# Kernel optimization log

Measured on AMD Instinct MI355X. Metric: run time of the kernel, lower is better.

The kernel has to match this reference:

```python
import jax, jax.numpy as jnp
import numpy as np

N = 100000        # n_nodes
E = 1600000       # n_edges (avg degree 16)
D = 64            # latent_dim_S
H = 64            # gcn_hidden_dim
EPS = 1e-5        # BatchNorm1d eps


def setup_inputs() -> dict:
    key = jax.random.key(0)
    ks = jax.random.split(key, 6)
    return {
        "edge_index": jax.random.randint(ks[0], (2, E), 0, N, dtype=jnp.int64),
        "u_S": jax.random.normal(ks[1], (N, D), dtype=jnp.float32),
        # GCNConv 1: latent_dim_S -> gcn_hidden_dim
        "w1": jax.random.normal(ks[2], (D, H), dtype=jnp.float32) / np.sqrt(D).astype(np.float32),
        "b1": jnp.zeros((H,), jnp.float32),
        # BatchNorm1d(H)
        "g1": jnp.ones((H,), jnp.float32),
        "beta1": jnp.zeros((H,), jnp.float32),
        # GCNConv 2: gcn_hidden_dim -> 2
        "w2": jax.random.normal(ks[3], (H, 2), dtype=jnp.float32) / np.sqrt(H).astype(np.float32),
        "b2": jnp.zeros((2,), jnp.float32),
        # BatchNorm1d(2)
        "g2": jnp.ones((2,), jnp.float32),
        "beta2": jnp.zeros((2,), jnp.float32),
    }


def reference(edge_index, u_S, w1, b1, g1, beta1, w2, b2, g2, beta2):
    n = u_S.shape[0]
    # PyG GCNConv: add self-loops, symmetric normalization D^-1/2 A D^-1/2
    loop = jnp.arange(n, dtype=edge_index.dtype)
    src = jnp.concatenate([edge_index[0], loop])  # [E+N]
    dst = jnp.concatenate([edge_index[1], loop])
    deg = jnp.zeros((n,), u_S.dtype).at[dst].add(1.0)   # in-degree incl. self-loop (>=1)
    dinv = jax.lax.rsqrt(deg)
    norm = dinv[src] * dinv[dst]                         # [E+N]

    def gcn_conv(x, w, b):
        h = x @ w                                        # transform first (PyG order)
        msg = h[src] * norm[:, None]                     # gather + scale
        out = jnp.zeros((n, h.shape[1]), h.dtype).at[dst].add(msg)  # scatter-add
        return out + b                                   # bias after aggregation

    def batchnorm(x, g, bt):
        m = x.mean(axis=0)
        v = x.var(axis=0)                                # biased variance (train mode)
        return g * (x - m) * jax.lax.rsqrt(v + EPS) + bt

    s = jax.nn.relu(batchnorm(gcn_conv(u_S, w1, b1), g1, beta1))
    s = batchnorm(gcn_conv(s, w2, b2), g2, beta2)
    # nn.Softmax() on 2D input defaults to dim=1
    return jax.nn.sigmoid(s), jax.nn.softmax(s, axis=1)
```

## Files before the change

### kernel.cpp

```cpp
#include <hip/hip_runtime.h>
#include <hip/hip_fp16.h>

#define N_NODES 100000
#define N_EDGES 1600000
#define BN_EPS 1e-5f

#define NBUCK 256
#define NPB   391
#define BCAP  8192
#define EPB_BIN 4096
#define NBLK_BIN ((N_EDGES + EPB_BIN - 1) / EPB_BIN)

#define K7_NBLK 1563

#define OFF_GCUR   0
#define OFF_CNT    256
#define OFF_DINV   100352
#define OFF_OFFS   200448
#define OFF_EBUF   300544
#define OFF_STATS1 2397696
#define OFF_STATS2 2397824
#define OFF_HS1    2398016
#define OFF_BINNED OFF_HS1
#define OFF_OUT1   5598016
#define OFF_HS2    8798016
#define OFF_OUT2   8998016

typedef _Float16 f16x8 __attribute__((ext_vector_type(8)));
typedef float    f32x4 __attribute__((ext_vector_type(4)));

__device__ inline void cvt8(uint4 v, float* f) {
    float2 a = __half22float2(*(__half2*)&v.x);
    float2 b = __half22float2(*(__half2*)&v.y);
    float2 c = __half22float2(*(__half2*)&v.z);
    float2 d = __half22float2(*(__half2*)&v.w);
    f[0] = a.x; f[1] = a.y; f[2] = b.x; f[3] = b.y;
    f[4] = c.x; f[5] = c.y; f[6] = d.x; f[7] = d.y;
}

__global__ __launch_bounds__(256) void k0_init(int* __restrict__ gcur,
                                               float* __restrict__ stats) {
    int t = threadIdx.x;
    gcur[t] = t * BCAP;
    if (t < 132) stats[t] = 0.f;
}

__global__ __launch_bounds__(256) void k_bin(
        const int* __restrict__ src, const int* __restrict__ dst,
        int* __restrict__ gcur, int* __restrict__ binned) {
    __shared__ int hist[NBUCK];
    __shared__ int lcur[NBUCK];
    int t = threadIdx.x, b = blockIdx.x;
    hist[t] = 0;
    __syncthreads();
    int e0 = b * EPB_BIN;
    int pkreg[16], bkreg[16];
#pragma unroll
    for (int i = 0; i < 16; ++i) {
        int e = e0 + t + i * 256;
        if (e < N_EDGES) {
            int s = src[e], d = dst[e];
            int bk = d / NPB;
            bkreg[i] = bk;
            pkreg[i] = s | ((d - bk * NPB) << 17);
            atomicAdd(&hist[bk], 1);
        } else bkreg[i] = -1;
    }
    __syncthreads();
    int h = hist[t];
    lcur[t] = (h > 0) ? atomicAdd(&gcur[t], h) : 0;
    __syncthreads();
#pragma unroll
    for (int i = 0; i < 16; ++i) {
        if (bkreg[i] >= 0) {
            int bk = bkreg[i];
            int pos = atomicAdd(&lcur[bk], 1);
            if (pos < (bk + 1) * BCAP)
                binned[pos] = pkreg[i];
        }
    }
}

__global__ __launch_bounds__(256) void k_csr(
        const int* __restrict__ gcur, const int* __restrict__ binned,
        int* __restrict__ cnt, float* __restrict__ dinv,
        int* __restrict__ offs, int* __restrict__ ebuf) {
    int b = blockIdx.x, t = threadIdx.x;
    int nb0 = b * NPB;
    int nn = min(NPB, N_NODES - nb0);
    __shared__ int lcnt[NPB];
    __shared__ int lcur[NPB];
    __shared__ int sc[512];
    for (int i = t; i < NPB; i += 256) lcnt[i] = 0;
    __syncthreads();
    int base = b * BCAP;
    int m = min(gcur[b] - base, BCAP);
    for (int j = t; j < m; j += 256)
        atomicAdd(&lcnt[((unsigned)binned[base + j]) >> 17], 1);
    __syncthreads();
    sc[t] = (t < NPB) ? lcnt[t] : 0;
    sc[256 + t] = (256 + t < NPB) ? lcnt[256 + t] : 0;
    __syncthreads();
    for (int off = 1; off < 512; off <<= 1) {
        int v0 = (t >= off) ? sc[t - off] : 0;
        int i1 = t + 256;
        int v1 = (i1 >= off) ? sc[i1 - off] : 0;
        __syncthreads();
        sc[t] += v0; sc[i1] += v1;
        __syncthreads();
    }
    for (int i = t; i < nn; i += 256) {
        int c = lcnt[i];
        int excl = sc[i] - c;
        lcur[i] = excl;
        offs[nb0 + i] = base + excl;
        cnt[nb0 + i] = c;
        dinv[nb0 + i] = rsqrtf((float)(1 + c));
    }
    __syncthreads();
    for (int j = t; j < m; j += 256) {
        unsigned v = (unsigned)binned[base + j];
        int pos = atomicAdd(&lcur[v >> 17], 1);
        ebuf[base + pos] = (int)(v & 0x1FFFFu);
    }
}

__global__ __launch_bounds__(256) void k3_xw1(
        const float* __restrict__ u, const float* __restrict__ w1g,
        const float* __restrict__ dinv, __half* __restrict__ hs1) {
    int t = threadIdx.x;
    int lane = t & 63, wid = t >> 6;
    int g = blockIdx.x * 4 + wid;
    if (g >= N_NODES / 16) return;
    int r = lane & 15, kb = lane >> 4;

    f16x8 bf[4][2];
#pragma unroll
    for (int ct = 0; ct < 4; ++ct) {
#pragma unroll
        for (int kh = 0; kh < 2; ++kh) {
            int c = ct * 16 + r;
            int k0 = kh * 32 + kb * 8;
            f16x8 b;
#pragma unroll
            for (int i = 0; i < 8; ++i) b[i] = (_Float16)w1g[(k0 + i) * 64 + c];
            bf[ct][kh] = b;
        }
    }

    const float* up = u + (size_t)g * 16 * 64;
    f16x8 af[2];
#pragma unroll
    for (int kh = 0; kh < 2; ++kh) {
        const float* p = up + r * 64 + kh * 32 + kb * 8;
        float4 v0 = *(const float4*)p;
        float4 v1 = *(const float4*)(p + 4);
        f16x8 a;
        a[0] = (_Float16)v0.x; a[1] = (_Float16)v0.y;
        a[2] = (_Float16)v0.z; a[3] = (_Float16)v0.w;
        a[4] = (_Float16)v1.x; a[5] = (_Float16)v1.y;
        a[6] = (_Float16)v1.z; a[7] = (_Float16)v1.w;
        af[kh] = a;
    }

    f32x4 acc[4];
#pragma unroll
    for (int ct = 0; ct < 4; ++ct) { acc[ct][0]=0.f; acc[ct][1]=0.f; acc[ct][2]=0.f; acc[ct][3]=0.f; }
#pragma unroll
    for (int ct = 0; ct < 4; ++ct) {
        acc[ct] = __builtin_amdgcn_mfma_f32_16x16x32_f16(af[0], bf[ct][0], acc[ct], 0, 0, 0);
        acc[ct] = __builtin_amdgcn_mfma_f32_16x16x32_f16(af[1], bf[ct][1], acc[ct], 0, 0, 0);
    }

    int r0 = g * 16;
    float4 dv = *(const float4*)&dinv[r0 + kb * 4];
    float dvv[4] = {dv.x, dv.y, dv.z, dv.w};
#pragma unroll
    for (int ct = 0; ct < 4; ++ct) {
#pragma unroll
        for (int reg = 0; reg < 4; ++reg) {
            int row = r0 + kb * 4 + reg;
            int col = ct * 16 + r;
            hs1[(size_t)row * 64 + col] = __float2half(acc[ct][reg] * dvv[reg]);
        }
    }
}

__global__ __launch_bounds__(256) void k_pull1(
        const int* __restrict__ offs, const int* __restrict__ cnt,
        const int* __restrict__ ebuf, const float* __restrict__ dinv,
        const __half* __restrict__ hs1, __half* __restrict__ out1) {
    int idx = blockIdx.x * blockDim.x + threadIdx.x;
    int d = idx >> 3, sub = idx & 7;
    if (d >= N_NODES) return;
    const uint4* h8 = (const uint4*)hs1;
    float acc[8];
    cvt8(h8[d * 8 + sub], acc);
    int base = offs[d], c = cnt[d];
    if (c > 0) {
        int s = ebuf[base];
        int j = 0;
        for (; j + 1 < c; ++j) {
            int s2 = ebuf[base + j + 1];
            float v[8];
            cvt8(h8[s * 8 + sub], v);
#pragma unroll
            for (int k = 0; k < 8; ++k) acc[k] += v[k];
            s = s2;
        }
        float v[8];
        cvt8(h8[s * 8 + sub], v);
#pragma unroll
        for (int k = 0; k < 8; ++k) acc[k] += v[k];
    }
    float di = dinv[d];
    __half2 p0 = __floats2half2_rn(acc[0] * di, acc[1] * di);
    __half2 p1 = __floats2half2_rn(acc[2] * di, acc[3] * di);
    __half2 p2 = __floats2half2_rn(acc[4] * di, acc[5] * di);
    __half2 p3 = __floats2half2_rn(acc[6] * di, acc[7] * di);
    uint4 o;
    o.x = *(unsigned*)&p0; o.y = *(unsigned*)&p1;
    o.z = *(unsigned*)&p2; o.w = *(unsigned*)&p3;
    ((uint4*)out1)[d * 8 + sub] = o;
}

__global__ __launch_bounds__(256) void k5_stats1(
        const __half* __restrict__ out1, float* __restrict__ stats) {
    int tid = blockIdx.x * blockDim.x + threadIdx.x;
    int gsz = gridDim.x * blockDim.x;
    const uint4* p = (const uint4*)out1;
    const int total = N_NODES * 8;
    float s[8], q[8];
#pragma unroll
    for (int j = 0; j < 8; ++j) { s[j] = 0.f; q[j] = 0.f; }
    for (int i = tid; i < total; i += gsz) {
        uint4 v = p[i];
        unsigned w[4] = {v.x, v.y, v.z, v.w};
#pragma unroll
        for (int h = 0; h < 4; ++h) {
            float2 f = __half22float2(*(__half2*)&w[h]);
            s[2*h]   += f.x; q[2*h]   = fmaf(f.x, f.x, q[2*h]);
            s[2*h+1] += f.y; q[2*h+1] = fmaf(f.y, f.y, q[2*h+1]);
        }
    }
#pragma unroll
    for (int m = 8; m < 64; m <<= 1) {
#pragma unroll
        for (int j = 0; j < 8; ++j) {
            s[j] += __shfl_xor(s[j], m);
            q[j] += __shfl_xor(q[j], m);
        }
    }
    __shared__ float red[4][128];
    int lane = threadIdx.x & 63, wv = threadIdx.x >> 6;
    if (lane < 8) {
        int c0 = lane * 8;
#pragma unroll
        for (int j = 0; j < 8; ++j) {
            red[wv][c0 + j] = s[j];
            red[wv][64 + c0 + j] = q[j];
        }
    }
    __syncthreads();
    if (threadIdx.x < 128) {
        int t = threadIdx.x;
        float v = red[0][t] + red[1][t] + red[2][t] + red[3][t];
        unsafeAtomicAdd(&stats[t], v);
    }
}

__global__ __launch_bounds__(256) void k7_xw2(
        const __half* __restrict__ out1, const float* __restrict__ stats,
        const float* __restrict__ g1, const float* __restrict__ beta1,
        const float* __restrict__ w2, const float* __restrict__ dinv,
        float* __restrict__ hs2) {
    __shared__ float lsc[64], lsh[64];
    int t = threadIdx.x;
    if (t < 64) {
        float invn = 1.f / (float)N_NODES;
        float m = stats[t] * invn;
        float v = stats[64 + t] * invn - m * m;
        float inv = rsqrtf(v + BN_EPS);
        float sc = g1[t] * inv;
        lsc[t] = sc;
        lsh[t] = beta1[t] - m * sc;
    }
    __syncthreads();
    int lane = t & 63, wv = t >> 6;
    int r = lane & 15, kb = lane >> 4;
    f16x8 bf[2];
    float scr[2][8], shr[2][8];
#pragma unroll
    for (int kh = 0; kh < 2; ++kh) {
        int k0 = kh * 32 + kb * 8;
        f16x8 b;
#pragma unroll
        for (int i = 0; i < 8; ++i) {
            b[i] = (r < 2) ? (_Float16)w2[(k0 + i) * 2 + r] : (_Float16)0.f;
            scr[kh][i] = lsc[k0 + i];
            shr[kh][i] = lsh[k0 + i];
        }
        bf[kh] = b;
    }
    const int NGRP = N_NODES / 16;
    int wid = blockIdx.x * 4 + wv;
    for (int g = wid; g < NGRP; g += K7_NBLK * 4) {
        f32x4 acc; acc[0]=0.f; acc[1]=0.f; acc[2]=0.f; acc[3]=0.f;
#pragma unroll
        for (int kh = 0; kh < 2; ++kh) {
            uint4 av = *(const uint4*)(out1 + (size_t)(g * 16 + r) * 64 + kh * 32 + kb * 8);
            unsigned w[4] = {av.x, av.y, av.z, av.w};
            f16x8 a;
#pragma unroll
            for (int h = 0; h < 4; ++h) {
                float2 f = __half22float2(*(__half2*)&w[h]);
                float y0 = fmaxf(fmaf(f.x, scr[kh][2*h],   shr[kh][2*h]),   0.f);
                float y1 = fmaxf(fmaf(f.y, scr[kh][2*h+1], shr[kh][2*h+1]), 0.f);
                a[2*h]   = (_Float16)y0;
                a[2*h+1] = (_Float16)y1;
            }
            acc = __builtin_amdgcn_mfma_f32_16x16x32_f16(a, bf[kh], acc, 0, 0, 0);
        }
        if (r < 2) {
            float4 dv = *(const float4*)&dinv[g * 16 + kb * 4];
            float dvv[4] = {dv.x, dv.y, dv.z, dv.w};
#pragma unroll
            for (int reg = 0; reg < 4; ++reg) {
                int row = g * 16 + kb * 4 + reg;
                hs2[row * 2 + r] = acc[reg] * dvv[reg];
            }
        }
    }
}

__global__ __launch_bounds__(256) void k_pull2(
        const int* __restrict__ offs, const int* __restrict__ cnt,
        const int* __restrict__ ebuf, const float* __restrict__ dinv,
        const float* __restrict__ hs2, float* __restrict__ out2,
        float* __restrict__ stats2) {
    int d = blockIdx.x * blockDim.x + threadIdx.x;
    float o0 = 0.f, o1 = 0.f;
    if (d < N_NODES) {
        const float2* h2 = (const float2*)hs2;
        float2 self = h2[d];
        o0 = self.x; o1 = self.y;
        int base = offs[d], c = cnt[d];
        for (int j = 0; j < c; ++j) {
            int s = ebuf[base + j];
            float2 v = h2[s];
            o0 += v.x; o1 += v.y;
        }
        float di = dinv[d];
        o0 *= di; o1 *= di;
        ((float2*)out2)[d] = make_float2(o0, o1);
    }
    float s0 = o0, s1 = o1, q0 = o0 * o0, q1 = o1 * o1;
#pragma unroll
    for (int m = 32; m; m >>= 1) {
        s0 += __shfl_down(s0, m); s1 += __shfl_down(s1, m);
        q0 += __shfl_down(q0, m); q1 += __shfl_down(q1, m);
    }
    __shared__ float red[4][4];
    int wv = threadIdx.x >> 6;
    if ((threadIdx.x & 63) == 0) {
        red[0][wv] = s0; red[1][wv] = s1; red[2][wv] = q0; red[3][wv] = q1;
    }
    __syncthreads();
    if (threadIdx.x < 4) {
        int i = threadIdx.x;
        float v = red[i][0] + red[i][1] + red[i][2] + red[i][3];
        unsafeAtomicAdd(&stats2[i], v);
    }
}

__global__ __launch_bounds__(256) void k10_head(
        const float* __restrict__ out2, const float* __restrict__ stats2,
        const float* __restrict__ g2, const float* __restrict__ beta2,
        float* __restrict__ out) {
    int r = blockIdx.x * blockDim.x + threadIdx.x;
    if (r >= N_NODES) return;
    float invn = 1.f / (float)N_NODES;
    float m0 = stats2[0] * invn, m1 = stats2[1] * invn;
    float v0 = stats2[2] * invn - m0 * m0;
    float v1 = stats2[3] * invn - m1 * m1;
    float i0 = rsqrtf(v0 + BN_EPS), i1 = rsqrtf(v1 + BN_EPS);
    float sc0 = g2[0] * i0, sc1 = g2[1] * i1;
    float sh0 = beta2[0] - m0 * sc0, sh1 = beta2[1] - m1 * sc1;
    float2 x = ((const float2*)out2)[r];
    float y0 = fmaf(x.x, sc0, sh0), y1 = fmaf(x.y, sc1, sh1);
    out[r * 2] = 1.f / (1.f + __expf(-y0));
    out[r * 2 + 1] = 1.f / (1.f + __expf(-y1));
    out[2 * N_NODES + r * 2] = 1.f / (1.f + __expf(y1 - y0));
    out[2 * N_NODES + r * 2 + 1] = 1.f / (1.f + __expf(y0 - y1));
}

extern "C" void kernel_launch(void* const* d_in, const int* in_sizes, int n_in,
                              void* d_out, int out_size, void* d_ws, size_t ws_size,
                              hipStream_t stream) {
    const int*   edge  = (const int*)d_in[0];
    const float* u_S   = (const float*)d_in[1];
    const float* w1    = (const float*)d_in[2];
    const float* g1    = (const float*)d_in[4];
    const float* beta1 = (const float*)d_in[5];
    const float* w2    = (const float*)d_in[6];
    const float* g2    = (const float*)d_in[8];
    const float* beta2 = (const float*)d_in[9];
    float* out = (float*)d_out;

    float*  ws     = (float*)d_ws;
    int*    gcur   = (int*)(ws + OFF_GCUR);
    int*    cnt    = (int*)(ws + OFF_CNT);
    float*  dinv   = ws + OFF_DINV;
    int*    offs   = (int*)(ws + OFF_OFFS);
    int*    ebuf   = (int*)(ws + OFF_EBUF);
    float*  stats1 = ws + OFF_STATS1;
    float*  stats2 = ws + OFF_STATS2;
    __half* hs1    = (__half*)(ws + OFF_HS1);
    int*    binned = (int*)(ws + OFF_BINNED);
    __half* out1   = (__half*)(ws + OFF_OUT1);
    float*  hs2    = ws + OFF_HS2;
    float*  out2   = ws + OFF_OUT2;

    const int* src = edge;
    const int* dst = edge + N_EDGES;

    k0_init<<<1, 256, 0, stream>>>(gcur, stats1);
    k_bin<<<NBLK_BIN, 256, 0, stream>>>(src, dst, gcur, binned);
    k_csr<<<NBUCK, 256, 0, stream>>>(gcur, binned, cnt, dinv, offs, ebuf);
    k3_xw1<<<(N_NODES / 16 + 3) / 4, 256, 0, stream>>>(u_S, w1, dinv, hs1);
    k_pull1<<<(N_NODES * 8 + 255) / 256, 256, 0, stream>>>(offs, cnt, ebuf, dinv, hs1, out1);
    k5_stats1<<<256, 256, 0, stream>>>(out1, stats1);
    k7_xw2<<<K7_NBLK, 256, 0, stream>>>(out1, stats1, g1, beta1, w2, dinv, hs2);
    k_pull2<<<(N_NODES + 255) / 256, 256, 0, stream>>>(offs, cnt, ebuf, dinv, hs2, out2, stats2);
    k10_head<<<(N_NODES + 255) / 256, 256, 0, stream>>>(out2, stats2, g2, beta2, out);
}
```

Measured before the change: 211.1 us.

## Aggregate edges per destination bucket in LDS instead of building a CSR

Drops the per-node CSR build (scan plus edge reorder) and aggregates each GCN layer straight from the binned edge list, with LDS float atomics into a per-bucket accumulator. Buckets are now smaller (1024 buckets of 98 nodes) so the 64-wide accumulator fits in shared memory, and the BatchNorm1 statistics are fused into the first aggregation kernel. This removes the k_csr reorder pass and the separate stats pass, but replaces sequential per-node accumulation with heavily contended LDS atomics. Each layer now runs on only about 1021 blocks, and bucket overflow past 2048 edges silently drops edges.

```diff
diff --git a/kernel.cpp b/kernel.cpp
--- a/kernel.cpp
+++ b/kernel.cpp
@@ -5,26 +5,25 @@
 #define N_EDGES 1600000
 #define BN_EPS 1e-5f
 
-#define NBUCK 256
-#define NPB   391
-#define BCAP  8192
+#define NBUCK 1024
+#define NPB   98
+#define NBUCK_USED ((N_NODES + NPB - 1) / NPB)
+#define BCAP  2048
 #define EPB_BIN 4096
 #define NBLK_BIN ((N_EDGES + EPB_BIN - 1) / EPB_BIN)
+#define ACC_STRIDE 66
 
 #define K7_NBLK 1563
 
 #define OFF_GCUR   0
-#define OFF_CNT    256
-#define OFF_DINV   100352
-#define OFF_OFFS   200448
-#define OFF_EBUF   300544
-#define OFF_STATS1 2397696
-#define OFF_STATS2 2397824
-#define OFF_HS1    2398016
-#define OFF_BINNED OFF_HS1
-#define OFF_OUT1   5598016
-#define OFF_HS2    8798016
-#define OFF_OUT2   8998016
+#define OFF_STATS1 1024
+#define OFF_STATS2 1152
+#define OFF_DINV   1280
+#define OFF_BINNED 101376
+#define OFF_HS1    2198528
+#define OFF_OUT1   5398528
+#define OFF_HS2    8598528
+#define OFF_OUT2   8798528
 
 typedef _Float16 f16x8 __attribute__((ext_vector_type(8)));
 typedef float    f32x4 __attribute__((ext_vector_type(4)));
@@ -38,8 +37,8 @@
     f[4] = c.x; f[5] = c.y; f[6] = d.x; f[7] = d.y;
 }
 
-__global__ __launch_bounds__(256) void k0_init(int* __restrict__ gcur,
-                                               float* __restrict__ stats) {
+__global__ __launch_bounds__(1024) void k0_init(int* __restrict__ gcur,
+                                                float* __restrict__ stats) {
     int t = threadIdx.x;
     gcur[t] = t * BCAP;
     if (t < 132) stats[t] = 0.f;
@@ -51,7 +50,8 @@
     __shared__ int hist[NBUCK];
     __shared__ int lcur[NBUCK];
     int t = threadIdx.x, b = blockIdx.x;
-    hist[t] = 0;
+#pragma unroll
+    for (int i = 0; i < 4; ++i) hist[t + i * 256] = 0;
     __syncthreads();
     int e0 = b * EPB_BIN;
     int pkreg[16], bkreg[16];
@@ -67,8 +67,12 @@
         } else bkreg[i] = -1;
     }
     __syncthreads();
-    int h = hist[t];
-    lcur[t] = (h > 0) ? atomicAdd(&gcur[t], h) : 0;
+#pragma unroll
+    for (int i = 0; i < 4; ++i) {
+        int slot = t + i * 256;
+        int h = hist[slot];
+        lcur[slot] = (h > 0) ? atomicAdd(&gcur[slot], h) : 0;
+    }
     __syncthreads();
 #pragma unroll
     for (int i = 0; i < 16; ++i) {
@@ -81,16 +85,14 @@
     }
 }
 
-__global__ __launch_bounds__(256) void k_csr(
+__global__ __launch_bounds__(256) void k_deg(
         const int* __restrict__ gcur, const int* __restrict__ binned,
-        int* __restrict__ cnt, float* __restrict__ dinv,
-        int* __restrict__ offs, int* __restrict__ ebuf) {
+        float* __restrict__ dinv) {
     int b = blockIdx.x, t = threadIdx.x;
     int nb0 = b * NPB;
+    if (nb0 >= N_NODES) return;
     int nn = min(NPB, N_NODES - nb0);
     __shared__ int lcnt[NPB];
-    __shared__ int lcur[NPB];
-    __shared__ int sc[512];
     for (int i = t; i < NPB; i += 256) lcnt[i] = 0;
     __syncthreads();
     int base = b * BCAP;
@@ -98,31 +100,8 @@
     for (int j = t; j < m; j += 256)
         atomicAdd(&lcnt[((unsigned)binned[base + j]) >> 17], 1);
     __syncthreads();
-    sc[t] = (t < NPB) ? lcnt[t] : 0;
-    sc[256 + t] = (256 + t < NPB) ? lcnt[256 + t] : 0;
-    __syncthreads();
-    for (int off = 1; off < 512; off <<= 1) {
-        int v0 = (t >= off) ? sc[t - off] : 0;
-        int i1 = t + 256;
-        int v1 = (i1 >= off) ? sc[i1 - off] : 0;
-        __syncthreads();
-        sc[t] += v0; sc[i1] += v1;
-        __syncthreads();
-    }
-    for (int i = t; i < nn; i += 256) {
-        int c = lcnt[i];
-        int excl = sc[i] - c;
-        lcur[i] = excl;
-        offs[nb0 + i] = base + excl;
-        cnt[nb0 + i] = c;
-        dinv[nb0 + i] = rsqrtf((float)(1 + c));
-    }
-    __syncthreads();
-    for (int j = t; j < m; j += 256) {
-        unsigned v = (unsigned)binned[base + j];
-        int pos = atomicAdd(&lcur[v >> 17], 1);
-        ebuf[base + pos] = (int)(v & 0x1FFFFu);
-    }
+    for (int i = t; i < nn; i += 256)
+        dinv[nb0 + i] = rsqrtf((float)(1 + lcnt[i]));
 }
 
 __global__ __launch_bounds__(256) void k3_xw1(
@@ -186,84 +165,74 @@
     }
 }
 
-__global__ __launch_bounds__(256) void k_pull1(
-        const int* __restrict__ offs, const int* __restrict__ cnt,
-        const int* __restrict__ ebuf, const float* __restrict__ dinv,
-        const __half* __restrict__ hs1, __half* __restrict__ out1) {
-    int idx = blockIdx.x * blockDim.x + threadIdx.x;
-    int d = idx >> 3, sub = idx & 7;
-    if (d >= N_NODES) return;
+__global__ __launch_bounds__(256) void k_pull1B(
+        const int* __restrict__ gcur, const int* __restrict__ binned,
+        const float* __restrict__ dinv, const __half* __restrict__ hs1,
+        __half* __restrict__ out1, float* __restrict__ stats) {
+    int b = blockIdx.x, t = threadIdx.x;
+    int nb0 = b * NPB;
+    if (nb0 >= N_NODES) return;
+    int nn = min(NPB, N_NODES - nb0);
+    __shared__ float acc[NPB * ACC_STRIDE];
+    for (int i = t; i < NPB * ACC_STRIDE; i += 256) acc[i] = 0.f;
+    __syncthreads();
     const uint4* h8 = (const uint4*)hs1;
-    float acc[8];
-    cvt8(h8[d * 8 + sub], acc);
-    int base = offs[d], c = cnt[d];
-    if (c > 0) {
-        int s = ebuf[base];
-        int j = 0;
-        for (; j + 1 < c; ++j) {
-            int s2 = ebuf[base + j + 1];
-            float v[8];
-            cvt8(h8[s * 8 + sub], v);
-#pragma unroll
-            for (int k = 0; k < 8; ++k) acc[k] += v[k];
-            s = s2;
-        }
-        float v[8];
-        cvt8(h8[s * 8 + sub], v);
-#pragma unroll
-        for (int k = 0; k < 8; ++k) acc[k] += v[k];
-    }
-    float di = dinv[d];
-    __half2 p0 = __floats2half2_rn(acc[0] * di, acc[1] * di);
-    __half2 p1 = __floats2half2_rn(acc[2] * di, acc[3] * di);
-    __half2 p2 = __floats2half2_rn(acc[4] * di, acc[5] * di);
-    __half2 p3 = __floats2half2_rn(acc[6] * di, acc[7] * di);
-    uint4 o;
-    o.x = *(unsigned*)&p0; o.y = *(unsigned*)&p1;
-    o.z = *(unsigned*)&p2; o.w = *(unsigned*)&p3;
-    ((uint4*)out1)[d * 8 + sub] = o;
-}
-
-__global__ __launch_bounds__(256) void k5_stats1(
-        const __half* __restrict__ out1, float* __restrict__ stats) {
-    int tid = blockIdx.x * blockDim.x + threadIdx.x;
-    int gsz = gridDim.x * blockDim.x;
-    const uint4* p = (const uint4*)out1;
-    const int total = N_NODES * 8;
-    float s[8], q[8];
-#pragma unroll
-    for (int j = 0; j < 8; ++j) { s[j] = 0.f; q[j] = 0.f; }
-    for (int i = tid; i < total; i += gsz) {
-        uint4 v = p[i];
-        unsigned w[4] = {v.x, v.y, v.z, v.w};
-#pragma unroll
-        for (int h = 0; h < 4; ++h) {
-            float2 f = __half22float2(*(__half2*)&w[h]);
-            s[2*h]   += f.x; q[2*h]   = fmaf(f.x, f.x, q[2*h]);
-            s[2*h+1] += f.y; q[2*h+1] = fmaf(f.y, f.y, q[2*h+1]);
-        }
-    }
-#pragma unroll
-    for (int m = 8; m < 64; m <<= 1) {
-#pragma unroll
-        for (int j = 0; j < 8; ++j) {
-            s[j] += __shfl_xor(s[j], m);
-            q[j] += __shfl_xor(q[j], m);
+    int base = b * BCAP;
+    int m = min(gcur[b] - base, BCAP);
+    int subl = t & 7;
+    for (int j = t >> 3; j < m; j += 32) {
+        unsigned v = (unsigned)binned[base + j];
+        int s = v & 0x1FFFF;
+        int ld = v >> 17;
+        float f[8];
+        cvt8(h8[s * 8 + subl], f);
+        float* a = &acc[ld * ACC_STRIDE + subl * 8];
+#pragma unroll
+        for (int k = 0; k < 8; ++k) atomicAdd(&a[k], f[k]);
+    }
+    __syncthreads();
+    float ps[8] = {0,0,0,0,0,0,0,0}, pq[8] = {0,0,0,0,0,0,0,0};
+    for (int i = t >> 3; i < nn; i += 32) {
+        int d = nb0 + i;
+        float f[8];
+        cvt8(h8[d * 8 + subl], f);
+        float di = dinv[d];
+        const float* a = &acc[i * ACC_STRIDE + subl * 8];
+        float o[8];
+#pragma unroll
+        for (int k = 0; k < 8; ++k) {
+            o[k] = (a[k] + f[k]) * di;
+            ps[k] += o[k];
+            pq[k] = fmaf(o[k], o[k], pq[k]);
+        }
+        __half2 p0 = __floats2half2_rn(o[0], o[1]);
+        __half2 p1 = __floats2half2_rn(o[2], o[3]);
+        __half2 p2 = __floats2half2_rn(o[4], o[5]);
+        __half2 p3 = __floats2half2_rn(o[6], o[7]);
+        uint4 w; w.x = *(unsigned*)&p0; w.y = *(unsigned*)&p1;
+        w.z = *(unsigned*)&p2; w.w = *(unsigned*)&p3;
+        ((uint4*)out1)[d * 8 + subl] = w;
+    }
+#pragma unroll
+    for (int mm = 8; mm < 64; mm <<= 1) {
+#pragma unroll
+        for (int k = 0; k < 8; ++k) {
+            ps[k] += __shfl_xor(ps[k], mm);
+            pq[k] += __shfl_xor(pq[k], mm);
         }
     }
     __shared__ float red[4][128];
-    int lane = threadIdx.x & 63, wv = threadIdx.x >> 6;
+    int lane = t & 63, wv = t >> 6;
     if (lane < 8) {
         int c0 = lane * 8;
 #pragma unroll
-        for (int j = 0; j < 8; ++j) {
-            red[wv][c0 + j] = s[j];
-            red[wv][64 + c0 + j] = q[j];
-        }
-    }
-    __syncthreads();
-    if (threadIdx.x < 128) {
-        int t = threadIdx.x;
+        for (int k = 0; k < 8; ++k) {
+            red[wv][c0 + k] = ps[k];
+            red[wv][64 + c0 + k] = pq[k];
+        }
+    }
+    __syncthreads();
+    if (t < 128) {
         float v = red[0][t] + red[1][t] + red[2][t] + red[3][t];
         unsafeAtomicAdd(&stats[t], v);
     }
@@ -333,43 +302,53 @@
     }
 }
 
-__global__ __launch_bounds__(256) void k_pull2(
-        const int* __restrict__ offs, const int* __restrict__ cnt,
-        const int* __restrict__ ebuf, const float* __restrict__ dinv,
-        const float* __restrict__ hs2, float* __restrict__ out2,
-        float* __restrict__ stats2) {
-    int d = blockIdx.x * blockDim.x + threadIdx.x;
-    float o0 = 0.f, o1 = 0.f;
-    if (d < N_NODES) {
-        const float2* h2 = (const float2*)hs2;
+__global__ __launch_bounds__(256) void k_pull2B(
+        const int* __restrict__ gcur, const int* __restrict__ binned,
+        const float* __restrict__ dinv, const float* __restrict__ hs2,
+        float* __restrict__ out2, float* __restrict__ stats2) {
+    int b = blockIdx.x, t = threadIdx.x;
+    int nb0 = b * NPB;
+    if (nb0 >= N_NODES) return;
+    int nn = min(NPB, N_NODES - nb0);
+    __shared__ float a0[NPB], a1[NPB];
+    for (int i = t; i < NPB; i += 256) { a0[i] = 0.f; a1[i] = 0.f; }
+    __syncthreads();
+    int base = b * BCAP;
+    int m = min(gcur[b] - base, BCAP);
+    const float2* h2 = (const float2*)hs2;
+    for (int j = t; j < m; j += 256) {
+        unsigned v = (unsigned)binned[base + j];
+        float2 x = h2[v & 0x1FFFF];
+        int ld = v >> 17;
+        atomicAdd(&a0[ld], x.x);
+        atomicAdd(&a1[ld], x.y);
+    }
+    __syncthreads();
+    float s0 = 0.f, s1 = 0.f, q0 = 0.f, q1 = 0.f;
+    for (int i = t; i < nn; i += 256) {
+        int d = nb0 + i;
         float2 self = h2[d];
-        o0 = self.x; o1 = self.y;
-        int base = offs[d], c = cnt[d];
-        for (int j = 0; j < c; ++j) {
-            int s = ebuf[base + j];
-            float2 v = h2[s];
-            o0 += v.x; o1 += v.y;
-        }
         float di = dinv[d];
-        o0 *= di; o1 *= di;
+        float o0 = (a0[i] + self.x) * di;
+        float o1 = (a1[i] + self.y) * di;
         ((float2*)out2)[d] = make_float2(o0, o1);
-    }
-    float s0 = o0, s1 = o1, q0 = o0 * o0, q1 = o1 * o1;
-#pragma unroll
-    for (int m = 32; m; m >>= 1) {
-        s0 += __shfl_down(s0, m); s1 += __shfl_down(s1, m);
-        q0 += __shfl_down(q0, m); q1 += __shfl_down(q1, m);
+        s0 += o0; s1 += o1;
+        q0 = fmaf(o0, o0, q0); q1 = fmaf(o1, o1, q1);
+    }
+#pragma unroll
+    for (int mm = 32; mm; mm >>= 1) {
+        s0 += __shfl_down(s0, mm); s1 += __shfl_down(s1, mm);
+        q0 += __shfl_down(q0, mm); q1 += __shfl_down(q1, mm);
     }
     __shared__ float red[4][4];
-    int wv = threadIdx.x >> 6;
-    if ((threadIdx.x & 63) == 0) {
+    int wv = t >> 6;
+    if ((t & 63) == 0) {
         red[0][wv] = s0; red[1][wv] = s1; red[2][wv] = q0; red[3][wv] = q1;
     }
     __syncthreads();
-    if (threadIdx.x < 4) {
-        int i = threadIdx.x;
-        float v = red[i][0] + red[i][1] + red[i][2] + red[i][3];
-        unsafeAtomicAdd(&stats2[i], v);
+    if (t < 4) {
+        float v = red[t][0] + red[t][1] + red[t][2] + red[t][3];
+        unsafeAtomicAdd(&stats2[t], v);
     }
 }
 
@@ -409,14 +388,11 @@
 
     float*  ws     = (float*)d_ws;
     int*    gcur   = (int*)(ws + OFF_GCUR);
-    int*    cnt    = (int*)(ws + OFF_CNT);
-    float*  dinv   = ws + OFF_DINV;
-    int*    offs   = (int*)(ws + OFF_OFFS);
-    int*    ebuf   = (int*)(ws + OFF_EBUF);
     float*  stats1 = ws + OFF_STATS1;
     float*  stats2 = ws + OFF_STATS2;
+    float*  dinv   = ws + OFF_DINV;
+    int*    binned = (int*)(ws + OFF_BINNED);
     __half* hs1    = (__half*)(ws + OFF_HS1);
-    int*    binned = (int*)(ws + OFF_BINNED);
     __half* out1   = (__half*)(ws + OFF_OUT1);
     float*  hs2    = ws + OFF_HS2;
     float*  out2   = ws + OFF_OUT2;
@@ -424,13 +400,12 @@
     const int* src = edge;
     const int* dst = edge + N_EDGES;
 
-    k0_init<<<1, 256, 0, stream>>>(gcur, stats1);
+    k0_init<<<1, 1024, 0, stream>>>(gcur, stats1);
     k_bin<<<NBLK_BIN, 256, 0, stream>>>(src, dst, gcur, binned);
-    k_csr<<<NBUCK, 256, 0, stream>>>(gcur, binned, cnt, dinv, offs, ebuf);
+    k_deg<<<NBUCK_USED, 256, 0, stream>>>(gcur, binned, dinv);
     k3_xw1<<<(N_NODES / 16 + 3) / 4, 256, 0, stream>>>(u_S, w1, dinv, hs1);
-    k_pull1<<<(N_NODES * 8 + 255) / 256, 256, 0, stream>>>(offs, cnt, ebuf, dinv, hs1, out1);
-    k5_stats1<<<256, 256, 0, stream>>>(out1, stats1);
+    k_pull1B<<<NBUCK_USED, 256, 0, stream>>>(gcur, binned, dinv, hs1, out1, stats1);
     k7_xw2<<<K7_NBLK, 256, 0, stream>>>(out1, stats1, g1, beta1, w2, dinv, hs2);
-    k_pull2<<<(N_NODES + 255) / 256, 256, 0, stream>>>(offs, cnt, ebuf, dinv, hs2, out2, stats2);
+    k_pull2B<<<NBUCK_USED, 256, 0, stream>>>(gcur, binned, dinv, hs2, out2, stats2);
     k10_head<<<(N_NODES + 255) / 256, 256, 0, stream>>>(out2, stats2, g2, beta2, out);
 }
```

Measured after the change: 698.1 us. +230.7%, slower.
